# Kernel tuning notes

Hardware: AMD Instinct MI355X
Metric: run time of the kernel (lower is better)

The kernel has to match this reference:

```python
import jax, jax.numpy as jnp
import numpy as np

H2 = 450
W = 1242
H = 375
N_PTS = 4_000_000


def setup_inputs() -> dict:
    key = jax.random.key(0)
    k1, k2, k3, k4, k5 = jax.random.split(key, 5)
    # lidar point cloud in velodyne frame (homogeneous): x forward, y left, z up
    u = jax.random.uniform(k1, (N_PTS, 3), dtype=jnp.float32)
    x = u[:, 0] * 78.0 + 2.0           # 2..80 m forward
    y = (u[:, 1] - 0.5) * 40.0         # -20..20 m lateral
    z = (u[:, 2] - 0.5) * 4.0 - 1.0    # -3..1 m vertical
    velo = jnp.stack([x, y, z, jnp.ones_like(x)], axis=1)
    # KITTI-like padded 4x4 intrinsic
    intrinsic = jnp.array([[721.5, 0.0, 609.5, 0.0],
                           [0.0, 721.5, 172.8, 0.0],
                           [0.0, 0.0, 1.0, 0.0],
                           [0.0, 0.0, 0.0, 1.0]], dtype=jnp.float32)
    # cam extrinsic ~ identity with small stereo baseline translation
    camExtrinsic = jnp.eye(4, dtype=jnp.float32).at[0, 3].set(-0.06)
    # velodyne -> camera rigid transform
    R = jnp.array([[0.0, -1.0, 0.0],
                   [0.0, 0.0, -1.0],
                   [1.0, 0.0, 0.0]], dtype=jnp.float32)
    t = jnp.array([0.0, -0.08, -0.27], dtype=jnp.float32)
    lidarExtrinsic = jnp.eye(4, dtype=jnp.float32).at[:3, :3].set(R).at[:3, 3].set(t)
    d = jax.random.uniform(k2, (H2, W), dtype=jnp.float32) * 78.0 + 2.0
    sel = jax.random.uniform(k3, (H2, W), dtype=jnp.float32) > 0.3
    interp_depth = jnp.where(sel, d, 0.0)
    return {"velo": velo, "intrinsic": intrinsic, "camExtrinsic": camExtrinsic,
            "lidarExtrinsic": lidarExtrinsic, "interp_depth": interp_depth,
            "h": H, "w": W}


def reference(velo, intrinsic, camExtrinsic, lidarExtrinsic, interp_depth, h, w):
    h2, wd = interp_depth.shape
    n = velo.shape[0]
    f32 = interp_depth.dtype

    P_cam = intrinsic @ camExtrinsic      # 4x4 projection to camera image
    P_lid = intrinsic @ lidarExtrinsic    # 4x4 projection to lidar image

    # project points into camera image
    vp = velo @ P_cam.T                    # [N,4]
    vz = vp[:, 2]
    vx = vp[:, 0] / vz
    vy = vp[:, 1] / vz
    onimg = (velo[:, 0] > 0) & (vx > 0) & (vx < w) & (vy > 0) & (vy < h)

    # project points into lidar image
    nv = velo @ P_lid.T                    # [N,4]
    nz = nv[:, 2]
    nx = nv[:, 0] / nz
    ny = nv[:, 1] / nz
    rnx = jnp.round(nx).astype(jnp.int32)
    rny = jnp.round(ny).astype(jnp.int32)
    nval = (rnx >= 0) & (rnx < w) & (rny >= 0) & (rny < h2) & (nz > 0) & onimg

    # dense interp-depth backprojection / reprojection, [h2, w]
    xxx, yyy = jnp.meshgrid(jnp.arange(wd, dtype=f32), jnp.arange(h2, dtype=f32), indexing='xy')
    d = interp_depth
    pts = jnp.stack([xxx * d, yyy * d, d, jnp.ones_like(d)], axis=-1)  # [h2,w,4]
    M = P_cam @ jnp.linalg.inv(P_lid)
    pp = jnp.einsum('hwk,jk->hwj', pts, M)                              # [h2,w,4]
    ppz = pp[..., 2]
    ppz_safe = jnp.where(ppz != 0, ppz, 1.0)
    ppx = pp[..., 0] / ppz_safe
    ppy = pp[..., 1] / ppz_safe
    interp_vals = jnp.stack([xxx, yyy, d, ppx, ppy, ppz, jnp.zeros_like(d)], axis=-1)
    img = jnp.where((d > 0)[..., None], interp_vals, 0.0)               # [h2,w,7]

    # scatter lidar points (overwrites interp entries where both present)
    idxrec = jnp.arange(n, dtype=f32)
    pvals = jnp.stack([nx, ny, nz, vx, vy, vz, idxrec], axis=1)         # [N,7]
    y_safe = jnp.where(nval, rny, h2)                                   # OOB -> dropped
    img = img.at[y_safe, rnx].set(pvals, mode='drop')

    org_mask = jnp.zeros((h2, wd), dtype=f32).at[y_safe, rnx].set(1.0, mode='drop')
    # NOTE: the custom CUDA occlusion pass (LidarFilterCuda.lidar_denoise) is
    # not reproducible; reference keeps the pre-denoise mask (identity filter).
    noocc_mask = org_mask

    pt_idx = img[:, :, 6].astype(jnp.int32)
    keep = noocc_mask == 1
    fi_idx = jnp.where(keep, pt_idx, n)                                 # OOB -> dropped
    filterIndicator = jnp.zeros((n,), dtype=jnp.int32).at[fi_idx.reshape(-1)].set(1, mode='drop')

    return img, noocc_mask, org_mask, filterIndicator
```

## Files before the change

kernel.cpp:

```cpp
#include <hip/hip_runtime.h>

#define H2C 450
#define WC 1242
#define HC 375
#define NPTS 4000000
#define NPIX (H2C * WC)
#define TPB 256
#define PBLK 2048
#define PTHREADS (PBLK * TPB)


__device__ __forceinline__ void mm4(float* o, const float* a, const float* b) {
#pragma unroll
    for (int i = 0; i < 4; i++)
#pragma unroll
        for (int j = 0; j < 4; j++) {
            float t = a[i * 4 + 0] * b[0 * 4 + j];
            t = fmaf(a[i * 4 + 1], b[1 * 4 + j], t);
            t = fmaf(a[i * 4 + 2], b[2 * 4 + j], t);
            t = fmaf(a[i * 4 + 3], b[3 * 4 + j], t);
            o[i * 4 + j] = t;
        }
}

__device__ void compute_mats(const float* K, const float* C, const float* L, float* out48) {
#pragma clang fp contract(off)
    float Pc[16], Pl[16], A[16], X[16], M[16];
    int piv[4];
    mm4(Pc, K, C);
    mm4(Pl, K, L);
#pragma unroll
    for (int k = 0; k < 16; k++) A[k] = Pl[k];

#pragma unroll
    for (int k = 0; k < 4; k++) {
        int p = k; float mx = fabsf(A[k * 4 + k]);
#pragma unroll
        for (int r = k + 1; r < 4; r++) {
            float v = fabsf(A[r * 4 + k]);
            if (v > mx) { mx = v; p = r; }
        }
        piv[k] = p;
#pragma unroll
        for (int r = k + 1; r < 4; r++) {
            bool sw = (p == r);
#pragma unroll
            for (int j = 0; j < 4; j++) {
                float tk = A[k * 4 + j], tr = A[r * 4 + j];
                A[k * 4 + j] = sw ? tr : tk;
                A[r * 4 + j] = sw ? tk : tr;
            }
        }
        float akk = A[k * 4 + k];
        if (fabsf(akk) >= 1.17549435e-38f) {
            float rr = 1.0f / akk;
#pragma unroll
            for (int r2 = k + 1; r2 < 4; r2++) A[r2 * 4 + k] = A[r2 * 4 + k] * rr;
        } else {
#pragma unroll
            for (int r2 = k + 1; r2 < 4; r2++) A[r2 * 4 + k] = A[r2 * 4 + k] / akk;
        }
#pragma unroll
        for (int r = k + 1; r < 4; r++) {
            float lik = A[r * 4 + k];
#pragma unroll
            for (int j = k + 1; j < 4; j++) A[r * 4 + j] = A[r * 4 + j] - lik * A[k * 4 + j];
        }
    }

#pragma unroll
    for (int k = 0; k < 16; k++) X[k] = 0.0f;
    X[0] = X[5] = X[10] = X[15] = 1.0f;
#pragma unroll
    for (int k = 0; k < 4; k++) {
        int p = piv[k];
#pragma unroll
        for (int r = k + 1; r < 4; r++) {
            bool sw = (p == r);
#pragma unroll
            for (int j = 0; j < 4; j++) {
                float tk = X[k * 4 + j], tr = X[r * 4 + j];
                X[k * 4 + j] = sw ? tr : tk;
                X[r * 4 + j] = sw ? tk : tr;
            }
        }
    }
#pragma unroll
    for (int j = 0; j < 4; j++) {
#pragma unroll
        for (int k = 0; k < 4; k++) {
            float xk = X[k * 4 + j];
#pragma unroll
            for (int r = k + 1; r < 4; r++) X[r * 4 + j] = X[r * 4 + j] - xk * A[r * 4 + k];
        }
#pragma unroll
        for (int k = 3; k >= 0; k--) {
            float xk = X[k * 4 + j] / A[k * 4 + k];
            X[k * 4 + j] = xk;
#pragma unroll
            for (int r = 0; r < k; r++) X[r * 4 + j] = X[r * 4 + j] - xk * A[r * 4 + k];
        }
    }
    mm4(M, Pc, X);
#pragma unroll
    for (int k = 0; k < 16; k++) { out48[k] = Pc[k]; out48[16 + k] = Pl[k]; out48[32 + k] = M[k]; }
}

__global__ void __launch_bounds__(TPB, 4)
point_k(const float4* __restrict__ velo, const float* __restrict__ K,
        const float* __restrict__ C, const float* __restrict__ L,
        int* __restrict__ winner, float* __restrict__ fi, float* __restrict__ gmats) {
    __shared__ float smats[48];
    if (threadIdx.x == 0) compute_mats(K, C, L, smats);
    __syncthreads();
    if (blockIdx.x == 0 && threadIdx.x < 48) gmats[threadIdx.x] = smats[threadIdx.x];
    float pc0 = smats[0],  pc1 = smats[1],  pc2 = smats[2],  pc3 = smats[3];
    float pc4 = smats[4],  pc5 = smats[5],  pc6 = smats[6],  pc7 = smats[7];
    float pc8 = smats[8],  pc9 = smats[9],  pc10 = smats[10], pc11 = smats[11];
    float pl0 = smats[16], pl1 = smats[17], pl2 = smats[18], pl3 = smats[19];
    float pl4 = smats[20], pl5 = smats[21], pl6 = smats[22], pl7 = smats[23];
    float pl8 = smats[24], pl9 = smats[25], pl10 = smats[26], pl11 = smats[27];

    int tid = blockIdx.x * TPB + threadIdx.x;
    for (int i = tid; i < NPTS; i += PTHREADS) {
        fi[i] = 0.0f;
        float4 v = velo[i];
        float vp0 = fmaf(v.w, pc3,  fmaf(v.z, pc2,  fmaf(v.y, pc1, v.x * pc0)));
        float vp1 = fmaf(v.w, pc7,  fmaf(v.z, pc6,  fmaf(v.y, pc5, v.x * pc4)));
        float vz  = fmaf(v.w, pc11, fmaf(v.z, pc10, fmaf(v.y, pc9, v.x * pc8)));
        float vx = vp0 / vz;
        float vy = vp1 / vz;
        bool onimg = (v.x > 0.f) && (vx > 0.f) && (vx < (float)WC) && (vy > 0.f) && (vy < (float)HC);
        float nv0 = fmaf(v.w, pl3,  fmaf(v.z, pl2,  fmaf(v.y, pl1, v.x * pl0)));
        float nv1 = fmaf(v.w, pl7,  fmaf(v.z, pl6,  fmaf(v.y, pl5, v.x * pl4)));
        float nz  = fmaf(v.w, pl11, fmaf(v.z, pl10, fmaf(v.y, pl9, v.x * pl8)));
        float nx = nv0 / nz;
        float ny = nv1 / nz;
        float rx = rintf(nx);
        float ry = rintf(ny);
        if (onimg && (nz > 0.f) && (rx >= 0.f) && (rx < (float)WC) && (ry >= 0.f) && (ry < (float)H2C)) {
            int px = (int)rx, py = (int)ry;
            atomicMax(&winner[py * WC + px], i);
        }
    }
}

__global__ void __launch_bounds__(TPB)
resolve_k(const float* __restrict__ depth, const float4* __restrict__ velo,
          const float* __restrict__ mats, const int* __restrict__ winner,
          float* __restrict__ img, float* __restrict__ noocc,
          float* __restrict__ org, float* __restrict__ fi) {
#pragma clang fp contract(off)
    __shared__ float srec[TPB * 7];
    int pb = blockIdx.x * TPB;
    int p = pb + threadIdx.x;
    int valid = NPIX - pb; if (valid > TPB) valid = TPB;
    float o0 = 0.f, o1 = 0.f, o2 = 0.f, o3 = 0.f, o4 = 0.f, o5 = 0.f, o6 = 0.f;
    if (p < NPIX) {
        int wi = winner[p];
        if (wi >= 0) {
            float4 v = velo[wi];
            const float* Pc = mats;
            const float* Pl = mats + 16;
            float vp0 = fmaf(v.w, Pc[3],  fmaf(v.z, Pc[2],  fmaf(v.y, Pc[1], v.x * Pc[0])));
            float vp1 = fmaf(v.w, Pc[7],  fmaf(v.z, Pc[6],  fmaf(v.y, Pc[5], v.x * Pc[4])));
            float vz  = fmaf(v.w, Pc[11], fmaf(v.z, Pc[10], fmaf(v.y, Pc[9], v.x * Pc[8])));
            float nv0 = fmaf(v.w, Pl[3],  fmaf(v.z, Pl[2],  fmaf(v.y, Pl[1], v.x * Pl[0])));
            float nv1 = fmaf(v.w, Pl[7],  fmaf(v.z, Pl[6],  fmaf(v.y, Pl[5], v.x * Pl[4])));
            float nz  = fmaf(v.w, Pl[11], fmaf(v.z, Pl[10], fmaf(v.y, Pl[9], v.x * Pl[8])));
            o0 = nv0 / nz; o1 = nv1 / nz; o2 = nz;
            o3 = vp0 / vz; o4 = vp1 / vz; o5 = vz;
            o6 = (float)wi;
            noocc[p] = 1.0f;
            org[p] = 1.0f;
            fi[wi] = 1.0f;
        } else {
            noocc[p] = 0.0f;
            org[p] = 0.0f;
            float d = depth[p];
            if (d > 0.0f) {
                int y = p / WC, x = p - y * WC;
                float fx = (float)x, fy = (float)y;
                const float* M = mats + 32;
                float p0 = fx * d, p1 = fy * d;
                float pp0 = ((p0 * M[0] + p1 * M[1]) + d * M[2]) + M[3];
                float pp1 = ((p0 * M[4] + p1 * M[5]) + d * M[6]) + M[7];
                float pp2 = ((p0 * M[8] + p1 * M[9]) + d * M[10]) + M[11];
                float zs = (pp2 != 0.0f) ? pp2 : 1.0f;
                o0 = fx; o1 = fy; o2 = d;
                o3 = pp0 / zs; o4 = pp1 / zs; o5 = pp2;
                o6 = 0.0f;
            }
        }
    }
    float* r = srec + threadIdx.x * 7;
    r[0] = o0; r[1] = o1; r[2] = o2; r[3] = o3; r[4] = o4; r[5] = o5; r[6] = o6;
    __syncthreads();
    float* obase = img + (size_t)pb * 7;
    int nfl = valid * 7;
    for (int k = threadIdx.x; k < nfl; k += TPB) obase[k] = srec[k];
}

extern "C" void kernel_launch(void* const* d_in, const int* in_sizes, int n_in,
                              void* d_out, int out_size, void* d_ws, size_t ws_size,
                              hipStream_t stream) {
    const float* velo  = (const float*)d_in[0];
    const float* K     = (const float*)d_in[1];
    const float* C     = (const float*)d_in[2];
    const float* L     = (const float*)d_in[3];
    const float* depth = (const float*)d_in[4];

    float* out   = (float*)d_out;
    float* img   = out;
    float* noocc = out + (size_t)NPIX * 7;
    float* org   = noocc + NPIX;
    float* fi    = org + NPIX;

    float* gmats = (float*)d_ws;
    int* winner  = (int*)((char*)d_ws + 256);

    hipMemsetAsync(winner, 0xFF, (size_t)NPIX * sizeof(int), stream);

    point_k<<<PBLK, TPB, 0, stream>>>((const float4*)velo, K, C, L, winner, fi, gmats);

    resolve_k<<<(NPIX + TPB - 1) / TPB, TPB, 0, stream>>>(depth, (const float4*)velo, gmats, winner,
                                                          img, noocc, org, fi);
}
```

Baseline: 34.47 us.

## Drop per-block serial matrix setup; compute projections via wave shuffles, four points per thread

```diff
diff --git a/kernel.cpp b/kernel.cpp
--- a/kernel.cpp
+++ b/kernel.cpp
@@ -6,8 +6,7 @@
 #define NPTS 4000000
 #define NPIX (H2C * WC)
 #define TPB 256
-#define PBLK 2048
-#define PTHREADS (PBLK * TPB)
+#define QTR (NPTS / 4)
 
 
 __device__ __forceinline__ void mm4(float* o, const float* a, const float* b) {
@@ -106,43 +105,60 @@
     for (int k = 0; k < 16; k++) { out48[k] = Pc[k]; out48[16 + k] = Pl[k]; out48[32 + k] = M[k]; }
 }
 
-__global__ void __launch_bounds__(TPB, 4)
+__device__ __forceinline__ void point_body(float4 v, const float* pc, const float* pl,
+                                           int* __restrict__ winner, int i) {
+    float vp0 = fmaf(v.w, pc[3],  fmaf(v.z, pc[2],  fmaf(v.y, pc[1], v.x * pc[0])));
+    float vp1 = fmaf(v.w, pc[7],  fmaf(v.z, pc[6],  fmaf(v.y, pc[5], v.x * pc[4])));
+    float vz  = fmaf(v.w, pc[11], fmaf(v.z, pc[10], fmaf(v.y, pc[9], v.x * pc[8])));
+    float vx = vp0 / vz;
+    float vy = vp1 / vz;
+    bool onimg = (v.x > 0.f) && (vx > 0.f) && (vx < (float)WC) && (vy > 0.f) && (vy < (float)HC);
+    float nv0 = fmaf(v.w, pl[3],  fmaf(v.z, pl[2],  fmaf(v.y, pl[1], v.x * pl[0])));
+    float nv1 = fmaf(v.w, pl[7],  fmaf(v.z, pl[6],  fmaf(v.y, pl[5], v.x * pl[4])));
+    float nz  = fmaf(v.w, pl[11], fmaf(v.z, pl[10], fmaf(v.y, pl[9], v.x * pl[8])));
+    float nx = nv0 / nz;
+    float ny = nv1 / nz;
+    float rx = rintf(nx);
+    float ry = rintf(ny);
+    if (onimg && (nz > 0.f) && (rx >= 0.f) && (rx < (float)WC) && (ry >= 0.f) && (ry < (float)H2C)) {
+        int px = (int)rx, py = (int)ry;
+        atomicMax(&winner[py * WC + px], i);
+    }
+}
+
+__global__ void __launch_bounds__(TPB)
 point_k(const float4* __restrict__ velo, const float* __restrict__ K,
-        const float* __restrict__ C, const float* __restrict__ L,
+        const float* __restrict__ C, const float* __restrict__ Lm,
         int* __restrict__ winner, float* __restrict__ fi, float* __restrict__ gmats) {
-    __shared__ float smats[48];
-    if (threadIdx.x == 0) compute_mats(K, C, L, smats);
-    __syncthreads();
-    if (blockIdx.x == 0 && threadIdx.x < 48) gmats[threadIdx.x] = smats[threadIdx.x];
-    float pc0 = smats[0],  pc1 = smats[1],  pc2 = smats[2],  pc3 = smats[3];
-    float pc4 = smats[4],  pc5 = smats[5],  pc6 = smats[6],  pc7 = smats[7];
-    float pc8 = smats[8],  pc9 = smats[9],  pc10 = smats[10], pc11 = smats[11];
-    float pl0 = smats[16], pl1 = smats[17], pl2 = smats[18], pl3 = smats[19];
-    float pl4 = smats[20], pl5 = smats[21], pl6 = smats[22], pl7 = smats[23];
-    float pl8 = smats[24], pl9 = smats[25], pl10 = smats[26], pl11 = smats[27];
-
-    int tid = blockIdx.x * TPB + threadIdx.x;
-    for (int i = tid; i < NPTS; i += PTHREADS) {
-        fi[i] = 0.0f;
-        float4 v = velo[i];
-        float vp0 = fmaf(v.w, pc3,  fmaf(v.z, pc2,  fmaf(v.y, pc1, v.x * pc0)));
-        float vp1 = fmaf(v.w, pc7,  fmaf(v.z, pc6,  fmaf(v.y, pc5, v.x * pc4)));
-        float vz  = fmaf(v.w, pc11, fmaf(v.z, pc10, fmaf(v.y, pc9, v.x * pc8)));
-        float vx = vp0 / vz;
-        float vy = vp1 / vz;
-        bool onimg = (v.x > 0.f) && (vx > 0.f) && (vx < (float)WC) && (vy > 0.f) && (vy < (float)HC);
-        float nv0 = fmaf(v.w, pl3,  fmaf(v.z, pl2,  fmaf(v.y, pl1, v.x * pl0)));
-        float nv1 = fmaf(v.w, pl7,  fmaf(v.z, pl6,  fmaf(v.y, pl5, v.x * pl4)));
-        float nz  = fmaf(v.w, pl11, fmaf(v.z, pl10, fmaf(v.y, pl9, v.x * pl8)));
-        float nx = nv0 / nz;
-        float ny = nv1 / nz;
-        float rx = rintf(nx);
-        float ry = rintf(ny);
-        if (onimg && (nz > 0.f) && (rx >= 0.f) && (rx < (float)WC) && (ry >= 0.f) && (ry < (float)H2C)) {
-            int px = (int)rx, py = (int)ry;
-            atomicMax(&winner[py * WC + px], i);
-        }
-    }
+    int i = blockIdx.x * TPB + threadIdx.x;
+    if (i == 0) compute_mats(K, C, Lm, gmats);
+    if (i >= QTR) return;
+    float4 va = velo[i];
+    float4 vb = velo[i + QTR];
+    float4 vc = velo[i + 2 * QTR];
+    float4 vd = velo[i + 3 * QTR];
+    fi[i] = 0.0f;
+    fi[i + QTR] = 0.0f;
+    fi[i + 2 * QTR] = 0.0f;
+    fi[i + 3 * QTR] = 0.0f;
+    int lane = threadIdx.x & 63;
+    int e = lane % 12;
+    const float* B = (lane >= 12) ? Lm : C;
+    int i4 = (e >> 2) * 4, j = e & 3;
+    float t = K[i4 + 0] * B[0 + j];
+    t = fmaf(K[i4 + 1], B[4 + j], t);
+    t = fmaf(K[i4 + 2], B[8 + j], t);
+    t = fmaf(K[i4 + 3], B[12 + j], t);
+    float pc[12], pl[12];
+#pragma unroll
+    for (int q = 0; q < 12; q++) pc[q] = __shfl(t, q, 64);
+#pragma unroll
+    for (int q = 0; q < 12; q++) pl[q] = __shfl(t, 12 + q, 64);
+
+    point_body(va, pc, pl, winner, i);
+    point_body(vb, pc, pl, winner, i + QTR);
+    point_body(vc, pc, pl, winner, i + 2 * QTR);
+    point_body(vd, pc, pl, winner, i + 3 * QTR);
 }
 
 __global__ void __launch_bounds__(TPB)
@@ -221,7 +237,8 @@
 
     hipMemsetAsync(winner, 0xFF, (size_t)NPIX * sizeof(int), stream);
 
-    point_k<<<PBLK, TPB, 0, stream>>>((const float4*)velo, K, C, L, winner, fi, gmats);
+    point_k<<<(QTR + TPB - 1) / TPB, TPB, 0, stream>>>((const float4*)velo, K, C, L,
+                                                       winner, fi, gmats);
 
     resolve_k<<<(NPIX + TPB - 1) / TPB, TPB, 0, stream>>>(depth, (const float4*)velo, gmats, winner,
                                                           img, noocc, org, fi);
```

After: 29.82 us. 13.5% less time.
